# Optimization experiments

Measured on AMD Instinct MI355X. Metric: run time of the kernel, lower is better.

Reference implementation:

```python
import jax, jax.numpy as jnp
import numpy as np

N = 100000   # nodes
E = 400000   # edges per relation
D = 256      # in_dim == out_dim
H = 8        # heads
DK = D // H  # 32
R = 2        # relations
SQRT_DK = float(np.sqrt(DK))


def setup_inputs() -> dict:
    key = jax.random.key(0)
    ks = jax.random.split(key, 16)
    s = 1.0 / np.sqrt(D)
    h = jax.random.normal(ks[0], (N, D), jnp.float32)
    src0 = jax.random.randint(ks[1], (E,), 0, N, jnp.int32)
    dst0 = jax.random.randint(ks[2], (E,), 0, N, jnp.int32)
    src1 = jax.random.randint(ks[3], (E,), 0, N, jnp.int32)
    dst1 = jax.random.randint(ks[4], (E,), 0, N, jnp.int32)
    Wk = jax.random.normal(ks[5], (D, D), jnp.float32) * s
    Wq = jax.random.normal(ks[6], (D, D), jnp.float32) * s
    Wv = jax.random.normal(ks[7], (D, D), jnp.float32) * s
    Wa = jax.random.normal(ks[8], (D, D), jnp.float32) * s
    bk = jnp.zeros((D,), jnp.float32)
    bq = jnp.zeros((D,), jnp.float32)
    bv = jnp.zeros((D,), jnp.float32)
    ba = jnp.zeros((D,), jnp.float32)
    ln_g = jnp.ones((D,), jnp.float32)
    ln_b = jnp.zeros((D,), jnp.float32)
    rel_pri = jnp.ones((R, H), jnp.float32)
    xav = float(np.sqrt(6.0 / (DK + DK)))  # xavier_uniform gain=1
    rel_att = jax.random.uniform(ks[9], (R, H, DK, DK), jnp.float32, -xav, xav)
    rel_msg = jax.random.uniform(ks[10], (R, H, DK, DK), jnp.float32, -xav, xav)
    return dict(h=h, src0=src0, dst0=dst0, src1=src1, dst1=dst1,
                Wk=Wk, bk=bk, Wq=Wq, bq=bq, Wv=Wv, bv=bv, Wa=Wa, ba=ba,
                ln_g=ln_g, ln_b=ln_b, rel_pri=rel_pri, rel_att=rel_att, rel_msg=rel_msg)


def _layernorm(x, g, b):
    m = jnp.mean(x, axis=-1, keepdims=True)
    v = jnp.mean(jnp.square(x - m), axis=-1, keepdims=True)
    return (x - m) * jax.lax.rsqrt(v + 1e-5) * g + b


def reference(h, src0, dst0, src1, dst1, Wk, bk, Wq, bq, Wv, bv, Wa, ba,
              ln_g, ln_b, rel_pri, rel_att, rel_msg):
    # per-type K/Q/V projections -> [N, H, DK]
    k = (h @ Wk + bk).reshape(N, H, DK)
    q = (h @ Wq + bq).reshape(N, H, DK)
    v = (h @ Wv + bv).reshape(N, H, DK)

    def rel_agg(r, src, dst):
        # per-relation transform (einsum 'bij,ijk->bik' in the original)
        kr = jnp.einsum('nhd,hde->nhe', k, rel_att[r])
        vr = jnp.einsum('nhd,hde->nhe', v, rel_msg[r])
        # v_dot_u: per-edge per-head dot product, scaled by relation_pri / sqrt(d_k)
        score = jnp.einsum('ehd,ehd->eh', q[dst], kr[src]) * rel_pri[r] / SQRT_DK  # [E, H]
        # edge_softmax normalized over incoming edges of each dst node
        m = jax.ops.segment_max(score, dst, num_segments=N)
        m = jnp.where(jnp.isfinite(m), m, 0.0)  # empty segments
        ex = jnp.exp(score - m[dst])
        den = jax.ops.segment_sum(ex, dst, num_segments=N)
        attn = ex / den[dst]  # [E, H]
        # u_mul_e + sum aggregation
        msg = vr[src] * attn[:, :, None]  # [E, H, DK]
        return jax.ops.segment_sum(msg, dst, num_segments=N)  # [N, H, DK]

    # cross_reducer='mean' over the two relations
    t = (rel_agg(0, src0, dst0) + rel_agg(1, src1, dst1)) * 0.5
    t = t.reshape(N, D)
    # output projection + residual + LayerNorm (dropout off / eval)
    out = _layernorm(t @ Wa + ba + h, ln_g, ln_b)
    return out
```

## Files before the change

kernel.cpp:

```cpp
#include <hip/hip_runtime.h>
#include <cstdint>
#include <cstddef>


#define NN 100000
#define EE 400000

static constexpr float INV_SQRT_DK = 0.17677669529663687f;

static constexpr size_t OFF_Q      = 0;
static constexpr size_t OFF_KV     = OFF_Q + (size_t)NN * 256;
static constexpr size_t OFF_UNION  = OFF_KV + (size_t)NN * 512;
static constexpr size_t OFF_BBUF   = OFF_UNION;
static constexpr size_t OFF_ROWPTR = OFF_UNION;
static constexpr size_t OFF_CURSOR = OFF_ROWPTR + NN;
static constexpr size_t OFF_SRCS   = OFF_CURSOR + NN;
static constexpr size_t OFF_BIAS   = OFF_UNION + 1000000;
static constexpr size_t OFF_BT     = OFF_BIAS + 1280;
static constexpr size_t OFF_END    = OFF_BT + (size_t)1536 * 512 / 2;

using bf16x8 = __attribute__((ext_vector_type(8))) __bf16;
using f32x4v = __attribute__((ext_vector_type(4))) float;
using u32x4  = __attribute__((ext_vector_type(4))) unsigned int;

static __device__ inline unsigned int bf_bits(__bf16 b) {
    union { __bf16 b; unsigned short u; } x; x.b = b; return (unsigned int)x.u;
}
static __device__ inline float bf2f(unsigned short u) {
    union { unsigned int u; float f; } x; x.u = ((unsigned int)u) << 16; return x.f;
}

#define GLOAD_LDS16(gsrc, ldst) \
    __builtin_amdgcn_global_load_lds((const __attribute__((address_space(1))) void*)(gsrc), \
                                     (__attribute__((address_space(3))) void*)(ldst), 16, 0, 0)

__global__ __launch_bounds__(256)
void zero_kernel(float4* __restrict__ p, long n4)
{
    const long stride = (long)gridDim.x * blockDim.x;
    for (long i = (long)blockIdx.x * blockDim.x + threadIdx.x; i < n4; i += stride)
        p[i] = make_float4(0.f, 0.f, 0.f, 0.f);
}

__global__ __launch_bounds__(256)
void build_B_kernel(const float* __restrict__ Wk, const float* __restrict__ Wq,
                    const float* __restrict__ Wv,
                    const float* __restrict__ bk, const float* __restrict__ bq,
                    const float* __restrict__ bv,
                    const float* __restrict__ rel_att, const float* __restrict__ rel_msg,
                    float* __restrict__ Bbuf, float* __restrict__ biasbuf)
{
    const int din = blockIdx.x;
    const int t   = threadIdx.x;
    __shared__ float wk[256], wv[256];
    wk[t] = Wk[din * 256 + t];
    wv[t] = Wv[din * 256 + t];
    __syncthreads();
    const int h = t >> 5, e = t & 31;
    Bbuf[(size_t)din * 1280 + t] = Wq[din * 256 + t];
    #pragma unroll
    for (int r = 0; r < 2; ++r) {
        const float* ra = rel_att + (size_t)((r * 8 + h) * 32) * 32 + e;
        const float* rm = rel_msg + (size_t)((r * 8 + h) * 32) * 32 + e;
        float sa = 0.f, sm = 0.f;
        #pragma unroll
        for (int dd = 0; dd < 32; ++dd) {
            sa = fmaf(wk[h * 32 + dd], ra[dd * 32], sa);
            sm = fmaf(wv[h * 32 + dd], rm[dd * 32], sm);
        }
        Bbuf[(size_t)din * 1280 + 256 + r * 512 + t]       = sa;
        Bbuf[(size_t)din * 1280 + 256 + r * 512 + 256 + t] = sm;
    }
    if (din == 0) {
        biasbuf[t] = bq[t];
        #pragma unroll
        for (int r = 0; r < 2; ++r) {
            float sa = 0.f, sm = 0.f;
            #pragma unroll
            for (int dd = 0; dd < 32; ++dd) {
                sa = fmaf(bk[h * 32 + dd], rel_att[(size_t)((r * 8 + h) * 32 + dd) * 32 + e], sa);
                sm = fmaf(bv[h * 32 + dd], rel_msg[(size_t)((r * 8 + h) * 32 + dd) * 32 + e], sm);
            }
            biasbuf[256 + r * 512 + t]       = sa;
            biasbuf[256 + r * 512 + 256 + t] = sm;
        }
    }
}

__global__ __launch_bounds__(256)
void conv_B_kernel(const float* __restrict__ Bbuf, const float* __restrict__ Wa,
                   unsigned short* __restrict__ BT)
{
    const int n = blockIdx.x;
    const int k = threadIdx.x;
    const float v = (n < 1280) ? Bbuf[(size_t)k * 1280 + n]
                               : Wa[(size_t)k * 256 + (n - 1280)];
    __bf16 hi = (__bf16)v;
    __bf16 lo = (__bf16)(v - (float)hi);
    BT[(size_t)n * 512 + k]       = (unsigned short)bf_bits(hi);
    BT[(size_t)n * 512 + 256 + k] = (unsigned short)bf_bits(lo);
}

__global__ __launch_bounds__(256)
void gemm_mfma(const float* __restrict__ A, int lda,
               const unsigned short* __restrict__ BT,
               const float* __restrict__ bias,
               float* __restrict__ Qout, unsigned short* __restrict__ KVout,
               int M, float alpha)
{
    __shared__ __align__(16) unsigned short AsB[128 * 64];
    __shared__ __align__(16) unsigned short BsB[2][128 * 64];
    const int tid = threadIdx.x;
    const int bn = blockIdx.x * 128;
    const int bm = blockIdx.y * 128;
    const int wid = tid >> 6;
    const int l   = tid & 63;
    const int wm  = (wid >> 1) * 64;
    const int wn  = (wid & 1) * 64;
    const int l15 = l & 15;
    const int k8  = (l >> 4) * 8;

    f32x4v acc[4][4];
    #pragma unroll
    for (int i = 0; i < 4; ++i)
        #pragma unroll
        for (int j = 0; j < 4; ++j)
            acc[i][j] = (f32x4v){0.f, 0.f, 0.f, 0.f};

    float4 rA[2][2];

    auto g_load_A = [&](int kb) {
        #pragma unroll
        for (int it = 0; it < 2; ++it) {
            const int s = it * 256 + tid;
            const int row = s >> 2, c8 = (s & 3) * 8;
            const float* base = A + (size_t)(bm + row) * lda + kb * 32 + c8;
            const bool ok = (bm + row) < M;
            rA[it][0] = ok ? *reinterpret_cast<const float4*>(base)     : make_float4(0,0,0,0);
            rA[it][1] = ok ? *reinterpret_cast<const float4*>(base + 4) : make_float4(0,0,0,0);
        }
    };
    auto stage_B = [&](int kb, int buf) {
        char* lbase = reinterpret_cast<char*>(&BsB[buf][0]);
        #pragma unroll
        for (int it = 0; it < 4; ++it) {
            const int s = it * 256 + tid;
            const int row = s >> 3, q = s & 7;
            const int qq = q ^ (row & 7);
            const char* gsrc = reinterpret_cast<const char*>(BT) + (size_t)(bn + row) * 1024
                               + ((qq < 4) ? (kb * 64 + qq * 16) : (512 + kb * 64 + (qq - 4) * 16));
            GLOAD_LDS16(gsrc, lbase + s * 16);
        }
    };

    stage_B(0, 0);
    g_load_A(0);

    for (int kb = 0; kb < 8; ++kb) {
        __syncthreads();
        #pragma unroll
        for (int it = 0; it < 2; ++it) {
            const int s = it * 256 + tid;
            const int row = s >> 2, c8 = (s & 3) * 8;
            float vv[8] = {rA[it][0].x, rA[it][0].y, rA[it][0].z, rA[it][0].w,
                           rA[it][1].x, rA[it][1].y, rA[it][1].z, rA[it][1].w};
            unsigned int hw[4], lw[4];
            #pragma unroll
            for (int j = 0; j < 4; ++j) {
                const __bf16 h0 = (__bf16)vv[2*j],  h1 = (__bf16)vv[2*j+1];
                const float  r0 = vv[2*j] - (float)h0, r1 = vv[2*j+1] - (float)h1;
                const __bf16 l0 = (__bf16)r0, l1 = (__bf16)r1;
                hw[j] = bf_bits(h0) | (bf_bits(h1) << 16);
                lw[j] = bf_bits(l0) | (bf_bits(l1) << 16);
            }
            const int swz = (row & 7) << 4;
            char* basep = reinterpret_cast<char*>(AsB);
            *reinterpret_cast<u32x4*>(basep + ((row * 128 +      c8 * 2) ^ swz)) = (u32x4){hw[0],hw[1],hw[2],hw[3]};
            *reinterpret_cast<u32x4*>(basep + ((row * 128 + 64 + c8 * 2) ^ swz)) = (u32x4){lw[0],lw[1],lw[2],lw[3]};
        }
        __syncthreads();
        if (kb < 7) { stage_B(kb + 1, (kb + 1) & 1); g_load_A(kb + 1); }

        const char* bbase = reinterpret_cast<const char*>(&BsB[kb & 1][0]);
        #pragma unroll
        for (int term = 0; term < 3; ++term) {
            const int apart = (term == 1) ? 64 : 0;
            const int bpart = (term == 2) ? 64 : 0;
            bf16x8 af[4], bfr[4];
            #pragma unroll
            for (int i = 0; i < 4; ++i) {
                const int arow = wm + i * 16 + l15;
                af[i]  = *reinterpret_cast<const bf16x8*>(reinterpret_cast<const char*>(AsB)
                           + ((arow * 128 + apart + k8 * 2) ^ ((arow & 7) << 4)));
                const int brow = wn + i * 16 + l15;
                bfr[i] = *reinterpret_cast<const bf16x8*>(bbase
                           + ((brow * 128 + bpart + k8 * 2) ^ ((brow & 7) << 4)));
            }
            #pragma unroll
            for (int i = 0; i < 4; ++i)
                #pragma unroll
                for (int j = 0; j < 4; ++j)
                    acc[i][j] = __builtin_amdgcn_mfma_f32_16x16x32_bf16(af[i], bfr[j], acc[i][j], 0, 0, 0);
        }
    }

    const bool q_seg = (bn < 256);
    #pragma unroll
    for (int i = 0; i < 4; ++i) {
        const int rbase = bm + wm + i * 16 + (l >> 4) * 4;
        #pragma unroll
        for (int j = 0; j < 4; ++j) {
            const int col = bn + wn + j * 16 + l15;
            const float bcol = bias[col];
            #pragma unroll
            for (int r = 0; r < 4; ++r) {
                const int row = rbase + r;
                if (row < M) {
                    const float o = alpha * acc[i][j][r] + bcol;
                    if (q_seg)
                        Qout[(size_t)row * 256 + col] = o;
                    else
                        KVout[(size_t)row * 1024 + (col - 256)] = (unsigned short)bf_bits((__bf16)o);
                }
            }
        }
    }
}

__global__ __launch_bounds__(256)
void hist2_kernel(const int* __restrict__ dst0, const int* __restrict__ dst1,
                  int* __restrict__ deg)
{
    const int stride = gridDim.x * blockDim.x;
    for (int i = blockIdx.x * blockDim.x + threadIdx.x; i < 2 * EE; i += stride) {
        const int d = (i < EE) ? dst0[i] : dst1[i - EE];
        atomicAdd(&deg[d], 1);
    }
}

__global__ __launch_bounds__(1024)
void scan1_kernel(const int* __restrict__ deg, int* __restrict__ rowptr,
                  int* __restrict__ part, int n)
{
    __shared__ int sm[1024];
    const int tid = threadIdx.x;
    const int i = blockIdx.x * 1024 + tid;
    const int v = (i < n) ? deg[i] : 0;
    sm[tid] = v;
    __syncthreads();
    for (int off = 1; off < 1024; off <<= 1) {
        int add = (tid >= off) ? sm[tid - off] : 0;
        __syncthreads();
        sm[tid] += add;
        __syncthreads();
    }
    if (i < n) rowptr[i] = sm[tid] - v;
    if (tid == 1023) part[blockIdx.x] = sm[1023];
}

__global__ __launch_bounds__(1024)
void scan2_kernel(int* __restrict__ part, int np)
{
    __shared__ int sm[1024];
    const int tid = threadIdx.x;
    const int v = (tid < np) ? part[tid] : 0;
    sm[tid] = v;
    __syncthreads();
    for (int off = 1; off < 1024; off <<= 1) {
        int add = (tid >= off) ? sm[tid - off] : 0;
        __syncthreads();
        sm[tid] += add;
        __syncthreads();
    }
    if (tid < np) part[tid] = sm[tid] - v;
}

__global__ __launch_bounds__(256)
void scan3_kernel(int* __restrict__ rowptr, int* __restrict__ cursor,
                  const int* __restrict__ part, int n)
{
    const int i = blockIdx.x * 256 + threadIdx.x;
    if (i < n) {
        const int r = rowptr[i] + part[i >> 10];
        rowptr[i] = r;
        cursor[i] = r;
    }
}

__global__ __launch_bounds__(256)
void scatter2_kernel(const int* __restrict__ src0, const int* __restrict__ dst0,
                     const int* __restrict__ src1, const int* __restrict__ dst1,
                     int* __restrict__ cursor, int* __restrict__ srcs)
{
    const int stride = gridDim.x * blockDim.x;
    for (int i = blockIdx.x * blockDim.x + threadIdx.x; i < 2 * EE; i += stride) {
        const int rel = (i >= EE);
        const int e = rel ? (i - EE) : i;
        const int d  = rel ? dst1[e] : dst0[e];
        const int sv = (rel ? src1[e] : src0[e]) | (rel << 20);
        int pos = atomicAdd(&cursor[d], 1);
        srcs[pos] = sv;
    }
}

__global__ __launch_bounds__(256)
void node_agg2_kernel(const float* __restrict__ Q, const unsigned short* __restrict__ KV,
                      const int* __restrict__ rowptr, const int* __restrict__ endptr,
                      const int* __restrict__ srcs,
                      const float* __restrict__ rel_pri,
                      float* __restrict__ AGG)
{
    const int node = (blockIdx.x * blockDim.x + threadIdx.x) >> 6;
    if (node >= NN) return;
    const int l = threadIdx.x & 63;
    const int h = l >> 3;
    const float4 q4 = reinterpret_cast<const float4*>(Q + (size_t)node * 256)[l];
    const float pr0 = rel_pri[h] * INV_SQRT_DK;
    const float pr1 = rel_pri[8 + h] * INV_SQRT_DK;
    const int s0 = rowptr[node];
    const int s1 = endptr[node];
    float m0 = -3.0e38f, m1 = -3.0e38f, den0 = 0.f, den1 = 0.f;
    float4 a0 = make_float4(0.f, 0.f, 0.f, 0.f);
    float4 a1 = make_float4(0.f, 0.f, 0.f, 0.f);
    for (int i = s0; i < s1; ++i) {
        const int p = srcs[i];
        const int s = p & 0xFFFFF;
        const int rel = p >> 20;
        const unsigned short* kv = KV + (size_t)s * 1024 + (rel << 9);
        const ushort4 k4 = *reinterpret_cast<const ushort4*>(kv + l * 4);
        float t = q4.x * bf2f(k4.x) + q4.y * bf2f(k4.y) + q4.z * bf2f(k4.z) + q4.w * bf2f(k4.w);
        t += __shfl_xor(t, 1, 64);
        t += __shfl_xor(t, 2, 64);
        t += __shfl_xor(t, 4, 64);
        const ushort4 v4 = *reinterpret_cast<const ushort4*>(kv + 256 + l * 4);
        const float vx = bf2f(v4.x), vy = bf2f(v4.y), vz = bf2f(v4.z), vw = bf2f(v4.w);
        if (rel == 0) {
            const float sc = t * pr0;
            const float mn = fmaxf(m0, sc);
            const float scale = __expf(m0 - mn);
            const float ex = __expf(sc - mn);
            den0 = den0 * scale + ex;
            a0.x = a0.x * scale + vx * ex;
            a0.y = a0.y * scale + vy * ex;
            a0.z = a0.z * scale + vz * ex;
            a0.w = a0.w * scale + vw * ex;
            m0 = mn;
        } else {
            const float sc = t * pr1;
            const float mn = fmaxf(m1, sc);
            const float scale = __expf(m1 - mn);
            const float ex = __expf(sc - mn);
            den1 = den1 * scale + ex;
            a1.x = a1.x * scale + vx * ex;
            a1.y = a1.y * scale + vy * ex;
            a1.z = a1.z * scale + vz * ex;
            a1.w = a1.w * scale + vw * ex;
            m1 = mn;
        }
    }
    const float i0 = (den0 > 0.f) ? 1.0f / den0 : 0.f;
    const float i1 = (den1 > 0.f) ? 1.0f / den1 : 0.f;
    float4 o;
    o.x = a0.x * i0 + a1.x * i1;
    o.y = a0.y * i0 + a1.y * i1;
    o.z = a0.z * i0 + a1.z * i1;
    o.w = a0.w * i0 + a1.w * i1;
    reinterpret_cast<float4*>(AGG + (size_t)node * 256)[l] = o;
}

__global__ __launch_bounds__(256)
void ln_kernel(const float* __restrict__ tmp, const float* __restrict__ hres,
               const float* __restrict__ g, const float* __restrict__ b,
               float* __restrict__ out, int M)
{
    const int gtid = blockIdx.x * blockDim.x + threadIdx.x;
    const int wid = gtid >> 6;
    const int nw = (gridDim.x * blockDim.x) >> 6;
    const int lane = threadIdx.x & 63;
    const float4 gv = reinterpret_cast<const float4*>(g)[lane];
    const float4 bv = reinterpret_cast<const float4*>(b)[lane];
    for (int row = wid; row < M; row += nw) {
        const float4 tv = reinterpret_cast<const float4*>(tmp + (size_t)row * 256)[lane];
        const float4 hv = reinterpret_cast<const float4*>(hres + (size_t)row * 256)[lane];
        float y0 = tv.x + hv.x, y1 = tv.y + hv.y, y2 = tv.z + hv.z, y3 = tv.w + hv.w;
        float ssum = y0 + y1 + y2 + y3;
        #pragma unroll
        for (int off = 32; off; off >>= 1) ssum += __shfl_xor(ssum, off, 64);
        const float mean = ssum * (1.f / 256.f);
        const float d0 = y0 - mean, d1 = y1 - mean, d2 = y2 - mean, d3 = y3 - mean;
        float sq = d0 * d0 + d1 * d1 + d2 * d2 + d3 * d3;
        #pragma unroll
        for (int off = 32; off; off >>= 1) sq += __shfl_xor(sq, off, 64);
        const float inv = rsqrtf(sq * (1.f / 256.f) + 1e-5f);
        float4 o;
        o.x = d0 * inv * gv.x + bv.x;
        o.y = d1 * inv * gv.y + bv.y;
        o.z = d2 * inv * gv.z + bv.z;
        o.w = d3 * inv * gv.w + bv.w;
        reinterpret_cast<float4*>(out + (size_t)row * 256)[lane] = o;
    }
}

extern "C" void kernel_launch(void* const* d_in, const int* in_sizes, int n_in,
                              void* d_out, int out_size, void* d_ws, size_t ws_size,
                              hipStream_t stream)
{
    const float* h    = (const float*)d_in[0];
    const int* src0   = (const int*)d_in[1];
    const int* dst0   = (const int*)d_in[2];
    const int* src1   = (const int*)d_in[3];
    const int* dst1   = (const int*)d_in[4];
    const float* Wk   = (const float*)d_in[5];
    const float* bk   = (const float*)d_in[6];
    const float* Wq   = (const float*)d_in[7];
    const float* bq   = (const float*)d_in[8];
    const float* Wv   = (const float*)d_in[9];
    const float* bv   = (const float*)d_in[10];
    const float* Wa   = (const float*)d_in[11];
    const float* ba   = (const float*)d_in[12];
    const float* lng  = (const float*)d_in[13];
    const float* lnb  = (const float*)d_in[14];
    const float* rel_pri = (const float*)d_in[15];
    const float* rel_att = (const float*)d_in[16];
    const float* rel_msg = (const float*)d_in[17];

    float* ws    = (float*)d_ws;
    float* Q     = ws + OFF_Q;
    unsigned short* KV = (unsigned short*)(ws + OFF_KV);
    float* BBUF  = ws + OFF_BBUF;
    float* BIAS  = ws + OFF_BIAS;
    int* ROWPTR  = (int*)(ws + OFF_ROWPTR);
    int* CURSOR  = (int*)(ws + OFF_CURSOR);
    int* SRCS    = (int*)(ws + OFF_SRCS);
    int* PART    = SRCS;
    unsigned short* BT = (unsigned short*)(ws + OFF_BT);
    float* AGG   = (float*)d_out;
    float* TMP   = ws + OFF_Q;

    const int NSCAN = (NN + 1023) / 1024;

    build_B_kernel<<<256, 256, 0, stream>>>(Wk, Wq, Wv, bk, bq, bv,
                                            rel_att, rel_msg, BBUF, BIAS);
    conv_B_kernel<<<1536, 256, 0, stream>>>(BBUF, Wa, BT);

    {
        dim3 grid(1280 / 128, (NN + 127) / 128);
        gemm_mfma<<<grid, 256, 0, stream>>>(h, 256, BT, BIAS, Q, KV, NN, 1.0f);
    }

    zero_kernel<<<128, 256, 0, stream>>>((float4*)CURSOR, (long)NN / 4);
    hist2_kernel<<<1024, 256, 0, stream>>>(dst0, dst1, CURSOR);
    scan1_kernel<<<NSCAN, 1024, 0, stream>>>(CURSOR, ROWPTR, PART, NN);
    scan2_kernel<<<1, 1024, 0, stream>>>(PART, NSCAN);
    scan3_kernel<<<(NN + 255) / 256, 256, 0, stream>>>(ROWPTR, CURSOR, PART, NN);
    scatter2_kernel<<<1024, 256, 0, stream>>>(src0, dst0, src1, dst1, CURSOR, SRCS);

    node_agg2_kernel<<<NN * 64 / 256, 256, 0, stream>>>(Q, KV, ROWPTR, CURSOR, SRCS,
                                                        rel_pri, AGG);

    {
        dim3 grid(256 / 128, (NN + 127) / 128);
        gemm_mfma<<<grid, 256, 0, stream>>>(AGG, 256, BT + (size_t)1280 * 512, ba,
                                            TMP, KV, NN, 0.5f);
    }
    ln_kernel<<<2048, 256, 0, stream>>>(TMP, h, lng, lnb, (float*)d_out, NN);
}
```

Measured before the change: 1.063 ms.

## Drop LDS staging in GEMM, load MFMA fragments directly, remap blocks per XCD

The MFMA GEMM no longer stages A and B tiles through shared memory with barriers. Each lane now loads its A and B fragments straight from global memory into registers, splits A into bf16 hi/lo in registers, and prefetches the next A slice. A 1D grid with XCD-aware block remapping is added so neighbouring tiles run on the same XCD for L2 reuse, launch bounds ask for 2 blocks per SIMD, and the edge loop in the aggregation kernel is unrolled by 2. The trade is losing LDS reuse across waves: each wave fetches its own fragments, so global and L2 traffic per block rises.

```diff
diff --git a/kernel.cpp b/kernel.cpp
--- a/kernel.cpp
+++ b/kernel.cpp
@@ -21,7 +21,6 @@
 
 using bf16x8 = __attribute__((ext_vector_type(8))) __bf16;
 using f32x4v = __attribute__((ext_vector_type(4))) float;
-using u32x4  = __attribute__((ext_vector_type(4))) unsigned int;
 
 static __device__ inline unsigned int bf_bits(__bf16 b) {
     union { __bf16 b; unsigned short u; } x; x.b = b; return (unsigned int)x.u;
@@ -29,10 +28,6 @@
 static __device__ inline float bf2f(unsigned short u) {
     union { unsigned int u; float f; } x; x.u = ((unsigned int)u) << 16; return x.f;
 }
-
-#define GLOAD_LDS16(gsrc, ldst) \
-    __builtin_amdgcn_global_load_lds((const __attribute__((address_space(1))) void*)(gsrc), \
-                                     (__attribute__((address_space(3))) void*)(ldst), 16, 0, 0)
 
 __global__ __launch_bounds__(256)
 void zero_kernel(float4* __restrict__ p, long n4)
@@ -101,18 +96,21 @@
     BT[(size_t)n * 512 + 256 + k] = (unsigned short)bf_bits(lo);
 }
 
-__global__ __launch_bounds__(256)
+__global__ __launch_bounds__(256, 2)
 void gemm_mfma(const float* __restrict__ A, int lda,
                const unsigned short* __restrict__ BT,
                const float* __restrict__ bias,
                float* __restrict__ Qout, unsigned short* __restrict__ KVout,
-               int M, float alpha)
-{
-    __shared__ __align__(16) unsigned short AsB[128 * 64];
-    __shared__ __align__(16) unsigned short BsB[2][128 * 64];
+               int M, int nbn, float alpha)
+{
+    const int nwg = gridDim.x;
+    const int q = nwg >> 3, r = nwg & 7;
+    const int xcd = blockIdx.x & 7, idx = blockIdx.x >> 3;
+    const int logical = (xcd < r ? xcd * (q + 1) : r * (q + 1) + (xcd - r) * q) + idx;
+    const int bn = (logical % nbn) * 128;
+    const int bm = (logical / nbn) * 128;
+
     const int tid = threadIdx.x;
-    const int bn = blockIdx.x * 128;
-    const int bm = blockIdx.y * 128;
     const int wid = tid >> 6;
     const int l   = tid & 63;
     const int wm  = (wid >> 1) * 64;
@@ -127,81 +125,76 @@
         for (int j = 0; j < 4; ++j)
             acc[i][j] = (f32x4v){0.f, 0.f, 0.f, 0.f};
 
-    float4 rA[2][2];
-
-    auto g_load_A = [&](int kb) {
-        #pragma unroll
-        for (int it = 0; it < 2; ++it) {
-            const int s = it * 256 + tid;
-            const int row = s >> 2, c8 = (s & 3) * 8;
-            const float* base = A + (size_t)(bm + row) * lda + kb * 32 + c8;
-            const bool ok = (bm + row) < M;
-            rA[it][0] = ok ? *reinterpret_cast<const float4*>(base)     : make_float4(0,0,0,0);
-            rA[it][1] = ok ? *reinterpret_cast<const float4*>(base + 4) : make_float4(0,0,0,0);
-        }
-    };
-    auto stage_B = [&](int kb, int buf) {
-        char* lbase = reinterpret_cast<char*>(&BsB[buf][0]);
-        #pragma unroll
-        for (int it = 0; it < 4; ++it) {
-            const int s = it * 256 + tid;
-            const int row = s >> 3, q = s & 7;
-            const int qq = q ^ (row & 7);
-            const char* gsrc = reinterpret_cast<const char*>(BT) + (size_t)(bn + row) * 1024
-                               + ((qq < 4) ? (kb * 64 + qq * 16) : (512 + kb * 64 + (qq - 4) * 16));
-            GLOAD_LDS16(gsrc, lbase + s * 16);
-        }
-    };
-
-    stage_B(0, 0);
-    g_load_A(0);
+    const float* Abase[4];
+    bool aok[4];
+    #pragma unroll
+    for (int i = 0; i < 4; ++i) {
+        const int grow = bm + wm + i * 16 + l15;
+        aok[i] = grow < M;
+        Abase[i] = A + (size_t)(aok[i] ? grow : 0) * lda + k8;
+    }
+    const unsigned short* Bbase[4];
+    #pragma unroll
+    for (int j = 0; j < 4; ++j)
+        Bbase[j] = BT + (size_t)(bn + wn + j * 16 + l15) * 512 + k8;
+
+    const float4 fz = make_float4(0.f, 0.f, 0.f, 0.f);
+    float4 ra0[4], ra1[4];
+    #pragma unroll
+    for (int i = 0; i < 4; ++i) {
+        float4 t0 = *reinterpret_cast<const float4*>(Abase[i]);
+        float4 t1 = *reinterpret_cast<const float4*>(Abase[i] + 4);
+        ra0[i] = aok[i] ? t0 : fz;
+        ra1[i] = aok[i] ? t1 : fz;
+    }
 
     for (int kb = 0; kb < 8; ++kb) {
-        __syncthreads();
-        #pragma unroll
-        for (int it = 0; it < 2; ++it) {
-            const int s = it * 256 + tid;
-            const int row = s >> 2, c8 = (s & 3) * 8;
-            float vv[8] = {rA[it][0].x, rA[it][0].y, rA[it][0].z, rA[it][0].w,
-                           rA[it][1].x, rA[it][1].y, rA[it][1].z, rA[it][1].w};
-            unsigned int hw[4], lw[4];
-            #pragma unroll
-            for (int j = 0; j < 4; ++j) {
-                const __bf16 h0 = (__bf16)vv[2*j],  h1 = (__bf16)vv[2*j+1];
-                const float  r0 = vv[2*j] - (float)h0, r1 = vv[2*j+1] - (float)h1;
-                const __bf16 l0 = (__bf16)r0, l1 = (__bf16)r1;
-                hw[j] = bf_bits(h0) | (bf_bits(h1) << 16);
-                lw[j] = bf_bits(l0) | (bf_bits(l1) << 16);
+        bf16x8 bfh[4], bfl[4];
+        #pragma unroll
+        for (int j = 0; j < 4; ++j)
+            bfh[j] = *reinterpret_cast<const bf16x8*>(Bbase[j] + kb * 32);
+        #pragma unroll
+        for (int j = 0; j < 4; ++j)
+            bfl[j] = *reinterpret_cast<const bf16x8*>(Bbase[j] + 256 + kb * 32);
+        bf16x8 afh[4], afl[4];
+        #pragma unroll
+        for (int i = 0; i < 4; ++i) {
+            const float v[8] = {ra0[i].x, ra0[i].y, ra0[i].z, ra0[i].w,
+                                ra1[i].x, ra1[i].y, ra1[i].z, ra1[i].w};
+            bf16x8 hh, ll;
+            #pragma unroll
+            for (int e = 0; e < 8; ++e) {
+                const __bf16 hb = (__bf16)v[e];
+                hh[e] = hb;
+                ll[e] = (__bf16)(v[e] - (float)hb);
             }
-            const int swz = (row & 7) << 4;
-            char* basep = reinterpret_cast<char*>(AsB);
-            *reinterpret_cast<u32x4*>(basep + ((row * 128 +      c8 * 2) ^ swz)) = (u32x4){hw[0],hw[1],hw[2],hw[3]};
-            *reinterpret_cast<u32x4*>(basep + ((row * 128 + 64 + c8 * 2) ^ swz)) = (u32x4){lw[0],lw[1],lw[2],lw[3]};
-        }
-        __syncthreads();
-        if (kb < 7) { stage_B(kb + 1, (kb + 1) & 1); g_load_A(kb + 1); }
-
-        const char* bbase = reinterpret_cast<const char*>(&BsB[kb & 1][0]);
-        #pragma unroll
-        for (int term = 0; term < 3; ++term) {
-            const int apart = (term == 1) ? 64 : 0;
-            const int bpart = (term == 2) ? 64 : 0;
-            bf16x8 af[4], bfr[4];
+            afh[i] = hh;
+            afl[i] = ll;
+        }
+        if (kb < 7) {
             #pragma unroll
             for (int i = 0; i < 4; ++i) {
-                const int arow = wm + i * 16 + l15;
-                af[i]  = *reinterpret_cast<const bf16x8*>(reinterpret_cast<const char*>(AsB)
-                           + ((arow * 128 + apart + k8 * 2) ^ ((arow & 7) << 4)));
-                const int brow = wn + i * 16 + l15;
-                bfr[i] = *reinterpret_cast<const bf16x8*>(bbase
-                           + ((brow * 128 + bpart + k8 * 2) ^ ((brow & 7) << 4)));
+                float4 t0 = *reinterpret_cast<const float4*>(Abase[i] + (kb + 1) * 32);
+                float4 t1 = *reinterpret_cast<const float4*>(Abase[i] + (kb + 1) * 32 + 4);
+                ra0[i] = aok[i] ? t0 : fz;
+                ra1[i] = aok[i] ? t1 : fz;
             }
-            #pragma unroll
-            for (int i = 0; i < 4; ++i)
-                #pragma unroll
-                for (int j = 0; j < 4; ++j)
-                    acc[i][j] = __builtin_amdgcn_mfma_f32_16x16x32_bf16(af[i], bfr[j], acc[i][j], 0, 0, 0);
-        }
+        }
+        #pragma unroll
+        for (int i = 0; i < 4; ++i)
+            #pragma unroll
+            for (int j = 0; j < 4; ++j)
+                acc[i][j] = __builtin_amdgcn_mfma_f32_16x16x32_bf16(afh[i], bfh[j], acc[i][j], 0, 0, 0);
+        #pragma unroll
+        for (int i = 0; i < 4; ++i)
+            #pragma unroll
+            for (int j = 0; j < 4; ++j)
+                acc[i][j] = __builtin_amdgcn_mfma_f32_16x16x32_bf16(afl[i], bfh[j], acc[i][j], 0, 0, 0);
+        #pragma unroll
+        for (int i = 0; i < 4; ++i)
+            #pragma unroll
+            for (int j = 0; j < 4; ++j)
+                acc[i][j] = __builtin_amdgcn_mfma_f32_16x16x32_bf16(afh[i], bfl[j], acc[i][j], 0, 0, 0);
     }
 
     const bool q_seg = (bn < 256);
@@ -213,10 +206,10 @@
             const int col = bn + wn + j * 16 + l15;
             const float bcol = bias[col];
             #pragma unroll
-            for (int r = 0; r < 4; ++r) {
-                const int row = rbase + r;
+            for (int rr = 0; rr < 4; ++rr) {
+                const int row = rbase + rr;
                 if (row < M) {
-                    const float o = alpha * acc[i][j][r] + bcol;
+                    const float o = alpha * acc[i][j][rr] + bcol;
                     if (q_seg)
                         Qout[(size_t)row * 256 + col] = o;
                     else
@@ -322,6 +315,7 @@
     float m0 = -3.0e38f, m1 = -3.0e38f, den0 = 0.f, den1 = 0.f;
     float4 a0 = make_float4(0.f, 0.f, 0.f, 0.f);
     float4 a1 = make_float4(0.f, 0.f, 0.f, 0.f);
+    #pragma unroll 2
     for (int i = s0; i < s1; ++i) {
         const int p = srcs[i];
         const int s = p & 0xFFFFF;
@@ -444,8 +438,8 @@
     conv_B_kernel<<<1536, 256, 0, stream>>>(BBUF, Wa, BT);
 
     {
-        dim3 grid(1280 / 128, (NN + 127) / 128);
-        gemm_mfma<<<grid, 256, 0, stream>>>(h, 256, BT, BIAS, Q, KV, NN, 1.0f);
+        const int nwg = 10 * ((NN + 127) / 128);
+        gemm_mfma<<<nwg, 256, 0, stream>>>(h, 256, BT, BIAS, Q, KV, NN, 10, 1.0f);
     }
 
     zero_kernel<<<128, 256, 0, stream>>>((float4*)CURSOR, (long)NN / 4);
@@ -459,9 +453,9 @@
                                                         rel_pri, AGG);
 
     {
-        dim3 grid(256 / 128, (NN + 127) / 128);
-        gemm_mfma<<<grid, 256, 0, stream>>>(AGG, 256, BT + (size_t)1280 * 512, ba,
-                                            TMP, KV, NN, 0.5f);
+        const int nwg = 2 * ((NN + 127) / 128);
+        gemm_mfma<<<nwg, 256, 0, stream>>>(AGG, 256, BT + (size_t)1280 * 512, ba,
+                                           TMP, KV, NN, 2, 0.5f);
     }
     ln_kernel<<<2048, 256, 0, stream>>>(TMP, h, lng, lnb, (float*)d_out, NN);
 }
```

Result: slower. 1.196 ms (+12.5%).
